# Kernel optimization log

Measured on AMD Instinct MI355X. Metric: run time of the kernel, lower is better.

The kernel has to match this reference:

```python
import jax, jax.numpy as jnp
from jax import lax
import numpy as np

B, S, G = 16, 384, 384
N = S + G
E_CHAR, D = 100, 128
H = D // 2              # LSTM hidden per direction
NHEAD, NHID = 4, 64
T = 21                  # crf_input_dim = label_alphabet.size() + 1
START, STOP = T - 2, T - 1
ALPHA = 0.2
CHAR_V, GAZ_V = 8000, 100000
NEG = -9e15             # pyGAT masked_fill value


def setup_inputs():
    key = jax.random.key(0)
    ks = jax.random.split(key, 20)
    f32 = jnp.float32
    def nrm(k, shape, s=0.05):
        return (jax.random.normal(k, shape) * s).astype(f32)
    eye = jnp.eye(N, dtype=bool)
    def adj(k):
        return ((jax.random.uniform(k, (B, N, N)) < 0.1) | eye[None]).astype(jnp.int32)
    return dict(
        batch_char=jax.random.randint(ks[0], (B, S), 0, CHAR_V),
        batch_len=jnp.full((B,), S, jnp.int32),
        gaz_list=jax.random.randint(ks[1], (B, G), 0, GAZ_V),
        t_graph=adj(ks[2]), c_graph=adj(ks[3]), l_graph=adj(ks[4]),
        mask=jnp.ones((B, S), jnp.int32),
        char_table=nrm(ks[5], (CHAR_V, E_CHAR)),
        gaz_table=nrm(ks[6], (GAZ_V, D)),
        w_ih_f=nrm(ks[7], (4 * H, E_CHAR)), w_hh_f=nrm(ks[8], (4 * H, H)),
        b_f=jnp.zeros((4 * H,), f32),
        w_ih_b=nrm(ks[9], (4 * H, E_CHAR)), w_hh_b=nrm(ks[10], (4 * H, H)),
        b_b=jnp.zeros((4 * H,), f32),
        h2h_W=nrm(ks[11], (T, D)), h2h_b=jnp.zeros((T,), f32),
        gat_Wh=nrm(ks[12], (3, NHEAD, D, NHID)),
        gat_ah=nrm(ks[13], (3, NHEAD, 2 * NHID)),
        gat_Wo=nrm(ks[14], (3, NHEAD * NHID, T)),
        gat_ao=nrm(ks[15], (3, 2 * T)),
        fuse_w=jnp.ones((4,), f32),
        transitions=nrm(ks[16], (T, T)),
    )


def _lstm_dir(x, w_ih, w_hh, b, reverse):
    # x: [B,S,E]; torch gate order i,f,g,o
    Bb = x.shape[0]
    Hh = w_hh.shape[1]
    xw = jnp.einsum('bse,ge->bsg', x, w_ih) + b
    def step(carry, xt):
        h, c = carry
        g = xt + h @ w_hh.T
        i, f, gg, o = jnp.split(g, 4, axis=-1)
        c = jax.nn.sigmoid(f) * c + jax.nn.sigmoid(i) * jnp.tanh(gg)
        h = jax.nn.sigmoid(o) * jnp.tanh(c)
        return (h, c), h
    h0 = jnp.zeros((Bb, Hh), x.dtype)
    _, hs = lax.scan(step, (h0, h0), xw.swapaxes(0, 1), reverse=reverse)
    return hs.swapaxes(0, 1)


def _gat_layer(x, adj, W, a, concat):
    # pyGAT batched layer: e_ij = LeakyReLU(a . [Wh_i || Wh_j]), masked softmax over j
    h = jnp.einsum('bnd,df->bnf', x, W)
    F_ = W.shape[1]
    f1 = h @ a[:F_]           # [B,N]
    f2 = h @ a[F_:]
    e = jax.nn.leaky_relu(f1[:, :, None] + f2[:, None, :], negative_slope=ALPHA)
    e = jnp.where(adj > 0, e, NEG)
    att = jax.nn.softmax(e, axis=-1)
    out = jnp.einsum('bij,bjf->bif', att, h)
    return jax.nn.elu(out) if concat else out


def _gat(x, adj, Wh, ah, Wo, ao):
    heads = jax.vmap(lambda W, a: _gat_layer(x, adj, W, a, True))(Wh, ah)  # [H,B,N,F]
    hcat = jnp.moveaxis(heads, 0, 2).reshape(x.shape[0], x.shape[1], -1)
    return jax.nn.elu(_gat_layer(hcat, adj, Wo, ao, False))


def _crf_feature(batch_char, gaz_list, graphs, char_table, gaz_table,
                 w_ih_f, w_hh_f, b_f, w_ih_b, w_hh_b, b_b, h2h_W, h2h_b,
                 gat_Wh, gat_ah, gat_Wo, gat_ao, fuse_w):
    emb = char_table[batch_char]                      # [B,S,E_CHAR]
    hf = _lstm_dir(emb, w_ih_f, w_hh_f, b_f, False)
    hb = _lstm_dir(emb, w_ih_b, w_hh_b, b_b, True)
    lstm_feat = jnp.concatenate([hf, hb], axis=-1)    # [B,S,D]
    gaz_feat = gaz_table[gaz_list]                    # [B,G,D]
    gat_in = jnp.concatenate([lstm_feat, gaz_feat], axis=1)  # [B,N,D]
    gat_outs = [_gat(gat_in, adj, gat_Wh[k], gat_ah[k], gat_Wo[k], gat_ao[k])[:, :S]
                for k, adj in enumerate(graphs)]
    lstm_proj = lstm_feat @ h2h_W.T + h2h_b           # [B,S,T]
    return (fuse_w[0] * lstm_proj + fuse_w[1] * gat_outs[0]
            + fuse_w[2] * gat_outs[1] + fuse_w[3] * gat_outs[2])


def _viterbi(feats, transitions, mask):
    Bb, Ss, Tt = feats.shape
    ids = jnp.arange(Tt)
    part0 = feats[:, 0, :] + transitions[START][None, :]
    def step(part, inp):
        feat_t, m_t = inp
        cur = part[:, :, None] + transitions[None] + feat_t[:, None, :]  # [B,prev,cur]
        new = cur.max(axis=1)
        bp = cur.argmax(axis=1)
        m = (m_t > 0)[:, None]
        return jnp.where(m, new, part), jnp.where(m, bp, ids[None, :])
    part, bps = lax.scan(step, part0,
                         (feats[:, 1:].swapaxes(0, 1), mask[:, 1:].swapaxes(0, 1)))
    last_tag = jnp.argmax(part + transitions[:, STOP][None, :], axis=1)
    def back(tag, bp):
        prev = jnp.take_along_axis(bp, tag[:, None], axis=1)[:, 0]
        return prev, prev
    _, prevs = lax.scan(back, last_tag, bps, reverse=True)   # prevs[j] = tag at time j
    return jnp.concatenate([prevs.swapaxes(0, 1), last_tag[:, None]], axis=1)


def reference(batch_char, batch_len, gaz_list, t_graph, c_graph, l_graph, mask,
              char_table, gaz_table, w_ih_f, w_hh_f, b_f, w_ih_b, w_hh_b, b_b,
              h2h_W, h2h_b, gat_Wh, gat_ah, gat_Wo, gat_ao, fuse_w, transitions):
    # batch_len is all == S (mask all ones), so packed BiLSTM == plain BiLSTM
    feats = _crf_feature(batch_char, gaz_list, (t_graph, c_graph, l_graph),
                         char_table, gaz_table, w_ih_f, w_hh_f, b_f,
                         w_ih_b, w_hh_b, b_b, h2h_W, h2h_b,
                         gat_Wh, gat_ah, gat_Wo, gat_ao, fuse_w)
    return _viterbi(feats, transitions, mask)
```

## Files before the change

### kernel.cpp

```cpp
#include <hip/hip_runtime.h>
#include <hip/hip_bf16.h>
#include <cstdint>
#include <cstddef>

#define BB 16
#define SS 384
#define GG 384
#define NN 768
#define DD 128
#define EC 100
#define TT 21
#define NHEADS 4
#define BN (BB*NN)
#define BS (BB*SS)

typedef float v2f __attribute__((ext_vector_type(2)));

__device__ __forceinline__ float sigf(float x) { return 1.0f / (1.0f + __expf(-x)); }
__device__ __forceinline__ float tanh_fast(float x) {
    return 1.0f - 2.0f / (__expf(2.0f * x) + 1.0f);
}
__device__ __forceinline__ float wred_max(float v) {
    #pragma unroll
    for (int o = 32; o > 0; o >>= 1) v = fmaxf(v, __shfl_xor(v, o));
    return v;
}
__device__ __forceinline__ float wred_sum(float v) {
    #pragma unroll
    for (int o = 32; o > 0; o >>= 1) v += __shfl_xor(v, o);
    return v;
}

__global__ __launch_bounds__(256) void k_xw(
    const int* __restrict__ batch_char, const float* __restrict__ char_table,
    const float* __restrict__ w_ih_f, const float* __restrict__ b_f,
    const float* __restrict__ w_ih_b, const float* __restrict__ b_b,
    float* __restrict__ xw_f, float* __restrict__ xw_b)
{
    __shared__ float At[EC * 68];
    __shared__ float Bt[EC * 68];
    __shared__ int   chs[64];
    const int tid = threadIdx.x;
    const int rt  = blockIdx.x;
    const int ot  = blockIdx.y;
    const int dir = ot >> 2, gt = ot & 3;
    const float* wih  = dir ? w_ih_b : w_ih_f;
    const float* bias = dir ? b_b    : b_f;
    float*       out  = dir ? xw_b   : xw_f;

    if (tid < 64) chs[tid] = batch_char[rt * 64 + tid];
    __syncthreads();
    for (int idx = tid; idx < 64 * EC; idx += 256) {
        int r = idx / EC, e = idx - r * EC;
        At[e * 68 + r] = char_table[(size_t)chs[r] * EC + e];
        Bt[e * 68 + r] = wih[(size_t)(gt * 64 + r) * EC + e];
    }
    __syncthreads();

    const int ty = tid >> 4, tx = tid & 15;
    const int r0 = ty * 4, c0 = tx * 4;
    float acc[4][4] = {};
    #pragma unroll 4
    for (int e = 0; e < EC; ++e) {
        float4 a = *(const float4*)&At[e * 68 + r0];
        float4 bv = *(const float4*)&Bt[e * 68 + c0];
        float av[4] = {a.x, a.y, a.z, a.w};
        float bb[4] = {bv.x, bv.y, bv.z, bv.w};
        #pragma unroll
        for (int i = 0; i < 4; ++i)
            #pragma unroll
            for (int j = 0; j < 4; ++j) acc[i][j] = fmaf(av[i], bb[j], acc[i][j]);
    }
    #pragma unroll
    for (int i = 0; i < 4; ++i) {
        int row = rt * 64 + r0 + i;
        int gc  = gt * 64 + c0;
        float4 o;
        o.x = acc[i][0] + bias[gc + 0];
        o.y = acc[i][1] + bias[gc + 1];
        o.z = acc[i][2] + bias[gc + 2];
        o.w = acc[i][3] + bias[gc + 3];
        *(float4*)&out[(size_t)row * 256 + gc] = o;
    }
}

__global__ __launch_bounds__(256) void k_gaz(
    const int* __restrict__ gaz_list, const float* __restrict__ gaz_table,
    float* __restrict__ gat_in)
{
    int idx = blockIdx.x * 256 + threadIdx.x;
    int d = idx & 127;
    int rest = idx >> 7;
    int g = rest % GG;
    int b = rest / GG;
    float v = gaz_table[(size_t)gaz_list[b * GG + g] * DD + d];
    gat_in[((size_t)b * NN + SS + g) * DD + d] = v;
}

__global__ __launch_bounds__(256) void k_lstm(
    const float* __restrict__ xw_f, const float* __restrict__ xw_b,
    const float* __restrict__ w_hh_f, const float* __restrict__ w_hh_b,
    float* __restrict__ gat_in)
{
    __shared__ float part[2][4][64][4];
    __shared__ float hbuf[4][64];
    const int tid = threadIdx.x, wv = tid >> 6, lane = tid & 63;
    const int b = blockIdx.x >> 1, dir = blockIdx.x & 1;
    const float* xw  = (dir ? xw_b : xw_f) + (size_t)b * SS * 256;
    const float* whh = dir ? w_hh_b : w_hh_f;
    v2f w2[4][8];
    #pragma unroll
    for (int g4 = 0; g4 < 4; ++g4) {
        const float* r = whh + (size_t)(g4 * 64 + lane) * 64 + 16 * wv;
        #pragma unroll
        for (int jj = 0; jj < 8; ++jj) w2[g4][jj] = v2f{r[2 * jj], r[2 * jj + 1]};
    }
    hbuf[wv][lane] = 0.f;
    float c = 0.f;
    int buf = 0;
    const int t0 = dir ? (SS - 1) : 0;
    float x0 = xw[t0 * 256 +   0 + lane];
    float x1 = xw[t0 * 256 +  64 + lane];
    float x2 = xw[t0 * 256 + 128 + lane];
    float x3 = xw[t0 * 256 + 192 + lane];
    const v2f* h2p = (const v2f*)&hbuf[wv][16 * wv];
    for (int tt = 0; tt < SS; ++tt) {
        const int t = dir ? (SS - 1 - tt) : tt;
        const int tn = dir ? (t - 1) : (t + 1);
        v2f a0 = v2f{0.f, 0.f}, a1 = v2f{0.f, 0.f}, a2 = v2f{0.f, 0.f}, a3 = v2f{0.f, 0.f};
        #pragma unroll
        for (int jj = 0; jj < 8; ++jj) {
            v2f hv = h2p[jj];
            a0 = __builtin_elementwise_fma(hv, w2[0][jj], a0);
            a1 = __builtin_elementwise_fma(hv, w2[1][jj], a1);
            a2 = __builtin_elementwise_fma(hv, w2[2][jj], a2);
            a3 = __builtin_elementwise_fma(hv, w2[3][jj], a3);
        }
        float4 pw;
        pw.x = a0.x + a0.y; pw.y = a1.x + a1.y;
        pw.z = a2.x + a2.y; pw.w = a3.x + a3.y;
        *(float4*)part[buf][wv][lane] = pw;
        float nx0 = 0.f, nx1 = 0.f, nx2 = 0.f, nx3 = 0.f;
        if (tt + 1 < SS) {
            nx0 = xw[tn * 256 +   0 + lane];
            nx1 = xw[tn * 256 +  64 + lane];
            nx2 = xw[tn * 256 + 128 + lane];
            nx3 = xw[tn * 256 + 192 + lane];
        }
        __syncthreads();
        float4 p0 = *(const float4*)part[buf][0][lane];
        float4 p1 = *(const float4*)part[buf][1][lane];
        float4 p2 = *(const float4*)part[buf][2][lane];
        float4 p3 = *(const float4*)part[buf][3][lane];
        float gi = ((p0.x + p1.x) + (p2.x + p3.x)) + x0;
        float gf = ((p0.y + p1.y) + (p2.y + p3.y)) + x1;
        float gg = ((p0.z + p1.z) + (p2.z + p3.z)) + x2;
        float go = ((p0.w + p1.w) + (p2.w + p3.w)) + x3;
        float nc = sigf(gf) * c + sigf(gi) * tanh_fast(gg);
        float nh = sigf(go) * tanh_fast(nc);
        c = nc;
        hbuf[wv][lane] = nh;
        if (wv == 0) gat_in[((size_t)b * NN + t) * DD + dir * 64 + lane] = nh;
        x0 = nx0; x1 = nx1; x2 = nx2; x3 = nx3;
        buf ^= 1;
    }
}

__global__ __launch_bounds__(256) void k_p1(
    const float* __restrict__ gat_in, const float* __restrict__ gat_Wh,
    const float* __restrict__ gat_ah, int k,
    float* __restrict__ h1, float* __restrict__ f1g, float* __restrict__ f2g)
{
    __shared__ float At[64 * 68];
    __shared__ float Bt[64 * 68];
    __shared__ float sf1[64], sf2[64];
    const int tid = threadIdx.x;
    const int rt = blockIdx.x, hd = blockIdx.y;
    if (tid < 64) { sf1[tid] = 0.f; sf2[tid] = 0.f; }
    const float* W = gat_Wh + ((size_t)(k * NHEADS + hd)) * DD * 64;
    const int ty = tid >> 4, tx = tid & 15;
    const int r0 = ty * 4, c0 = tx * 4;
    float acc[4][4] = {};
    for (int ph = 0; ph < 2; ++ph) {
        __syncthreads();
        for (int idx = tid; idx < 64 * 64; idx += 256) {
            int r = idx >> 6, e = idx & 63;
            At[e * 68 + r] = gat_in[((size_t)(rt * 64 + r)) * DD + ph * 64 + e];
            Bt[e * 68 + r] = W[(size_t)(ph * 64 + e) * 64 + r];
        }
        __syncthreads();
        #pragma unroll 4
        for (int e = 0; e < 64; ++e) {
            float4 a = *(const float4*)&At[e * 68 + r0];
            float4 bv = *(const float4*)&Bt[e * 68 + c0];
            float av[4] = {a.x, a.y, a.z, a.w};
            float bb[4] = {bv.x, bv.y, bv.z, bv.w};
            #pragma unroll
            for (int i = 0; i < 4; ++i)
                #pragma unroll
                for (int j = 0; j < 4; ++j) acc[i][j] = fmaf(av[i], bb[j], acc[i][j]);
        }
    }
    const float* ah = gat_ah + (size_t)(k * NHEADS + hd) * 128;
    float a1[4], a2[4];
    #pragma unroll
    for (int j = 0; j < 4; ++j) { a1[j] = ah[c0 + j]; a2[j] = ah[64 + c0 + j]; }
    #pragma unroll
    for (int i = 0; i < 4; ++i) {
        int n = rt * 64 + r0 + i;
        float4 o = make_float4(acc[i][0], acc[i][1], acc[i][2], acc[i][3]);
        *(float4*)&h1[((size_t)n * NHEADS + hd) * 64 + c0] = o;
        float p1 = acc[i][0] * a1[0] + acc[i][1] * a1[1] + acc[i][2] * a1[2] + acc[i][3] * a1[3];
        float p2 = acc[i][0] * a2[0] + acc[i][1] * a2[1] + acc[i][2] * a2[2] + acc[i][3] * a2[3];
        atomicAdd(&sf1[r0 + i], p1);
        atomicAdd(&sf2[r0 + i], p2);
    }
    __syncthreads();
    if (tid < 64) {
        f1g[hd * BN + rt * 64 + tid] = sf1[tid];
        f2g[hd * BN + rt * 64 + tid] = sf2[tid];
    }
}

__global__ __launch_bounds__(256) void k_attn1(
    const int* __restrict__ adj, const float* __restrict__ h1,
    const float* __restrict__ f1g, const float* __restrict__ f2g,
    float* __restrict__ out1, unsigned long long* __restrict__ packed)
{
    __shared__ int   nbr[NN];
    __shared__ float ep[NHEADS][NN];
    __shared__ unsigned long long wm[12];
    __shared__ int cntS;
    const int tid = threadIdx.x, wave = tid >> 6, lane = tid & 63;
    const int n = blockIdx.x;
    const int b = n / NN;
    #pragma unroll
    for (int it = 0; it < 3; ++it) {
        int j = it * 256 + tid;
        int a = adj[(size_t)n * NN + j];
        unsigned long long m = __ballot(a > 0);
        if (lane == 0) { wm[it * 4 + wave] = m; packed[(size_t)n * 12 + it * 4 + wave] = m; }
    }
    __syncthreads();
    if (wave == 0) {
        unsigned long long m = (lane < 12) ? wm[lane] : 0ULL;
        int pc = __popcll(m);
        int inc = pc;
        #pragma unroll
        for (int d = 1; d < 16; d <<= 1) { int t = __shfl_up(inc, d); if (lane >= d) inc += t; }
        int C = __shfl(inc, 11);
        if (lane == 0) cntS = C;
        int off = inc - pc;
        while (m) {
            int bit = __builtin_ctzll(m);
            nbr[off++] = lane * 64 + bit;
            m &= m - 1;
        }
    }
    __syncthreads();
    const int C = cntS;
    const int hd = wave;
    const float f1 = f1g[hd * BN + n];
    const float* f2p = f2g + hd * BN + b * NN;
    float mx = -3.0e38f;
    for (int t = lane; t < C; t += 64) {
        float e = f1 + f2p[nbr[t]];
        e = (e >= 0.f) ? e : 0.2f * e;
        ep[hd][t] = e;
        mx = fmaxf(mx, e);
    }
    mx = wred_max(mx);
    float sum = 0.f;
    for (int t = lane; t < C; t += 64) {
        float p = __expf(ep[hd][t] - mx);
        ep[hd][t] = p;
        sum += p;
    }
    sum = wred_sum(sum);
    const float* hb = h1 + (size_t)b * NN * (NHEADS * 64) + hd * 64 + lane;
    float ac0 = 0.f, ac1 = 0.f, ac2 = 0.f, ac3 = 0.f;
    int t = 0;
    for (; t + 3 < C; t += 4) {
        int j0 = nbr[t], j1 = nbr[t + 1], j2 = nbr[t + 2], j3 = nbr[t + 3];
        float p0 = ep[hd][t], p1 = ep[hd][t + 1], p2 = ep[hd][t + 2], p3 = ep[hd][t + 3];
        ac0 = fmaf(p0, hb[(size_t)j0 * 256], ac0);
        ac1 = fmaf(p1, hb[(size_t)j1 * 256], ac1);
        ac2 = fmaf(p2, hb[(size_t)j2 * 256], ac2);
        ac3 = fmaf(p3, hb[(size_t)j3 * 256], ac3);
    }
    for (; t < C; ++t) ac0 = fmaf(ep[hd][t], hb[(size_t)nbr[t] * 256], ac0);
    float r = ((ac0 + ac1) + (ac2 + ac3)) / sum;
    r = (r > 0.f) ? r : expm1f(r);
    out1[(size_t)n * 256 + hd * 64 + lane] = r;
}

__global__ __launch_bounds__(256) void k_p2(
    const float* __restrict__ out1, const float* __restrict__ gat_Wo,
    const float* __restrict__ gat_ao, int k,
    float* __restrict__ h2, float* __restrict__ f1o, float* __restrict__ f2o)
{
    __shared__ float ld[12 * 256];
    __shared__ float lf1[12], lf2[12];
    const int tid = threadIdx.x;
    const int blk = blockIdx.x;
    if (tid < 12) { lf1[tid] = 0.f; lf2[tid] = 0.f; }
    for (int idx = tid; idx < 12 * 256; idx += 256)
        ld[idx] = out1[(size_t)blk * 12 * 256 + idx];
    __syncthreads();
    if (tid < 252) {
        const int r = tid / TT, c = tid - r * TT;
        const float* Wo = gat_Wo + (size_t)k * 256 * TT;
        const float4* row4 = (const float4*)&ld[r * 256];
        float acc = 0.f;
        #pragma unroll 8
        for (int q4 = 0; q4 < 64; ++q4) {
            float4 v = row4[q4];
            int q = q4 * 4;
            acc = fmaf(v.x, Wo[(q + 0) * TT + c], acc);
            acc = fmaf(v.y, Wo[(q + 1) * TT + c], acc);
            acc = fmaf(v.z, Wo[(q + 2) * TT + c], acc);
            acc = fmaf(v.w, Wo[(q + 3) * TT + c], acc);
        }
        const int n = blk * 12 + r;
        h2[(size_t)n * TT + c] = acc;
        const float* ao = gat_ao + k * 2 * TT;
        atomicAdd(&lf1[r], acc * ao[c]);
        atomicAdd(&lf2[r], acc * ao[TT + c]);
    }
    __syncthreads();
    if (tid < 12) {
        f1o[blk * 12 + tid] = lf1[tid];
        f2o[blk * 12 + tid] = lf2[tid];
    }
}

__global__ __launch_bounds__(64) void k_attn2(
    const unsigned long long* __restrict__ packed,
    const float* __restrict__ h2, const float* __restrict__ f1o,
    const float* __restrict__ f2o, float* __restrict__ out2k)
{
    __shared__ int   nbr[NN];
    __shared__ float ep[NN];
    const int lane = threadIdx.x;
    const int blk = blockIdx.x;
    const int b = blk / SS, s = blk - b * SS;
    const int n = b * NN + s;
    unsigned long long w64 = (lane < 12) ? packed[(size_t)n * 12 + lane] : 0ULL;
    int pc = __popcll(w64);
    int inc = pc;
    #pragma unroll
    for (int d = 1; d < 16; d <<= 1) {
        int t = __shfl_up(inc, d, 16);
        if ((lane & 15) >= d) inc += t;
    }
    const int C = __shfl(inc, 11);
    int off = inc - pc;
    while (w64) {
        int bit = __builtin_ctzll(w64);
        nbr[off++] = lane * 64 + bit;
        w64 &= w64 - 1;
    }
    __syncthreads();
    const float f1 = f1o[n];
    const float* f2p = f2o + b * NN;
    float mx = -3.0e38f;
    for (int t = lane; t < C; t += 64) {
        int j = nbr[t];
        float e = f1 + f2p[j];
        e = (e >= 0.f) ? e : 0.2f * e;
        ep[t] = e;
        mx = fmaxf(mx, e);
    }
    mx = wred_max(mx);
    float sum = 0.f;
    for (int t = lane; t < C; t += 64) {
        float p = __expf(ep[t] - mx);
        ep[t] = p;
        sum += p;
    }
    sum = wred_sum(sum);
    const float* h2b = h2 + (size_t)b * NN * TT + ((lane < TT) ? lane : 0);
    float ac0 = 0.f, ac1 = 0.f, ac2 = 0.f, ac3 = 0.f;
    int t = 0;
    for (; t + 3 < C; t += 4) {
        int j0 = nbr[t], j1 = nbr[t + 1], j2 = nbr[t + 2], j3 = nbr[t + 3];
        float p0 = ep[t], p1 = ep[t + 1], p2 = ep[t + 2], p3 = ep[t + 3];
        ac0 = fmaf(p0, h2b[(size_t)j0 * TT], ac0);
        ac1 = fmaf(p1, h2b[(size_t)j1 * TT], ac1);
        ac2 = fmaf(p2, h2b[(size_t)j2 * TT], ac2);
        ac3 = fmaf(p3, h2b[(size_t)j3 * TT], ac3);
    }
    for (; t < C; ++t) ac0 = fmaf(ep[t], h2b[(size_t)nbr[t] * TT], ac0);
    if (lane < TT) {
        float r = ((ac0 + ac1) + (ac2 + ac3)) / sum;
        r = (r > 0.f) ? r : expm1f(r);
        out2k[(size_t)blk * TT + lane] = r;
    }
}

__global__ __launch_bounds__(64) void k_fuse(
    const float* __restrict__ gat_in, const float* __restrict__ h2h_W,
    const float* __restrict__ h2h_b, const float* __restrict__ fuse_w,
    const float* __restrict__ out2, float* __restrict__ feats)
{
    __shared__ float row[DD];
    const int lane = threadIdx.x;
    const int blk = blockIdx.x;
    const int b = blk / SS, s = blk - b * SS;
    const float* src = gat_in + ((size_t)b * NN + s) * DD;
    row[lane] = src[lane];
    row[lane + 64] = src[lane + 64];
    __syncthreads();
    if (lane < TT) {
        float acc = h2h_b[lane];
        const float4* w4 = (const float4*)&h2h_W[lane * DD];
        const float4* r4 = (const float4*)row;
        #pragma unroll 8
        for (int d4 = 0; d4 < 32; ++d4) {
            float4 w = w4[d4]; float4 v = r4[d4];
            acc = fmaf(w.x, v.x, acc); acc = fmaf(w.y, v.y, acc);
            acc = fmaf(w.z, v.z, acc); acc = fmaf(w.w, v.w, acc);
        }
        size_t o = (size_t)blk * TT + lane;
        feats[o] = fuse_w[0] * acc + fuse_w[1] * out2[o]
                 + fuse_w[2] * out2[(size_t)BS * TT + o]
                 + fuse_w[3] * out2[2 * (size_t)BS * TT + o];
    }
}

__global__ __launch_bounds__(64) void k_vit(
    const float* __restrict__ feats, const float* __restrict__ trans,
    int* __restrict__ out)
{
    __shared__ float part[24];
    __shared__ unsigned char bp[SS - 1][24];
    const int lane = threadIdx.x;
    const int b = blockIdx.x;
    const int pg = lane / TT;
    const int c = lane - pg * TT;
    const bool act = (pg < 3);
    const int p0 = pg * 7;
    float tc[7];
    if (act) {
        #pragma unroll
        for (int u = 0; u < 7; ++u) tc[u] = trans[(p0 + u) * TT + c];
    }
    if (lane < TT) part[lane] = feats[((size_t)b * SS) * TT + lane] + trans[19 * TT + lane];
    if (lane >= TT && lane < 24) part[lane] = -3.0e38f;
    __syncthreads();
    for (int t = 1; t < SS; ++t) {
        float best = -3.0e38f; int bi = 0;
        if (act) {
            #pragma unroll
            for (int u = 0; u < 7; ++u) {
                float v = part[p0 + u] + tc[u];
                if (v > best) { best = v; bi = p0 + u; }
            }
        }
        float bv1 = __shfl(best, lane + 21);
        int   bi1 = __shfl(bi,   lane + 21);
        float bv2 = __shfl(best, lane + 42);
        int   bi2 = __shfl(bi,   lane + 42);
        if (lane < TT) {
            if (bv1 > best) { best = bv1; bi = bi1; }
            if (bv2 > best) { best = bv2; bi = bi2; }
            bp[t - 1][lane] = (unsigned char)bi;
            part[lane] = best + feats[((size_t)b * SS + t) * TT + lane];
        }
        __syncthreads();
    }
    float fv = (lane < TT) ? part[lane] + trans[lane * TT + 20] : -3.0e38f;
    int fi = (lane < TT) ? lane : 0;
    #pragma unroll
    for (int o = 32; o > 0; o >>= 1) {
        float ov = __shfl_xor(fv, o);
        int oi = __shfl_xor(fi, o);
        if (ov > fv || (ov == fv && oi < fi)) { fv = ov; fi = oi; }
    }
    __syncthreads();
    if (lane == 0) {
        int cur = fi;
        out[b * SS + SS - 1] = cur;
        for (int u = SS - 2; u >= 0; --u) {
            cur = bp[u][cur];
            out[b * SS + u] = cur;
        }
    }
}

extern "C" void kernel_launch(void* const* d_in, const int* in_sizes, int n_in,
                              void* d_out, int out_size, void* d_ws, size_t ws_size,
                              hipStream_t stream) {
    (void)in_sizes; (void)n_in; (void)out_size; (void)ws_size;
    const int*   batch_char = (const int*)d_in[0];
    const int*   gaz_list   = (const int*)d_in[2];
    const int*   graphs[3]  = {(const int*)d_in[3], (const int*)d_in[4], (const int*)d_in[5]};
    const float* char_table = (const float*)d_in[7];
    const float* gaz_table  = (const float*)d_in[8];
    const float* w_ih_f = (const float*)d_in[9];
    const float* w_hh_f = (const float*)d_in[10];
    const float* b_f    = (const float*)d_in[11];
    const float* w_ih_b = (const float*)d_in[12];
    const float* w_hh_b = (const float*)d_in[13];
    const float* b_b    = (const float*)d_in[14];
    const float* h2h_W  = (const float*)d_in[15];
    const float* h2h_b  = (const float*)d_in[16];
    const float* gat_Wh = (const float*)d_in[17];
    const float* gat_ah = (const float*)d_in[18];
    const float* gat_Wo = (const float*)d_in[19];
    const float* gat_ao = (const float*)d_in[20];
    const float* fuse_w = (const float*)d_in[21];
    const float* trans  = (const float*)d_in[22];

    float* ws = (float*)d_ws;
    float* gat_in = ws;
    float* xw_f   = gat_in + 1572864;
    float* xw_b   = xw_f   + 1572864;
    float* h1     = xw_b   + 1572864;
    float* out1   = h1     + 3145728;
    float* h2     = out1   + 3145728;
    float* f1g    = h2     + 258048;
    float* f2g    = f1g    + 49152;
    float* f1o    = f2g    + 49152;
    float* f2o    = f1o    + 12288;
    float* out2   = f2o    + 12288;
    float* feats  = out2   + 387072;
    unsigned long long* packed = (unsigned long long*)(feats + 129024);

    k_xw<<<dim3(96, 8), 256, 0, stream>>>(batch_char, char_table, w_ih_f, b_f,
                                          w_ih_b, b_b, xw_f, xw_b);
    k_gaz<<<3072, 256, 0, stream>>>(gaz_list, gaz_table, gat_in);
    k_lstm<<<32, 256, 0, stream>>>(xw_f, xw_b, w_hh_f, w_hh_b, gat_in);
    for (int k = 0; k < 3; ++k) {
        k_p1<<<dim3(192, 4), 256, 0, stream>>>(gat_in, gat_Wh, gat_ah, k, h1, f1g, f2g);
        k_attn1<<<BN, 256, 0, stream>>>(graphs[k], h1, f1g, f2g, out1, packed);
        k_p2<<<1024, 256, 0, stream>>>(out1, gat_Wo, gat_ao, k, h2, f1o, f2o);
        k_attn2<<<BS, 64, 0, stream>>>(packed, h2, f1o, f2o, out2 + (size_t)k * BS * TT);
    }
    k_fuse<<<BS, 64, 0, stream>>>(gat_in, h2h_W, h2h_b, fuse_w, out2, feats);
    k_vit<<<BB, 64, 0, stream>>>(feats, trans, (int*)d_out);
}
```

Before: 948.6 us.

## Run LSTM recurrence in a single wavefront using readlane broadcasts

The BiLSTM recurrence kernel moves from four wavefronts that split the hidden-state dot product and combine partial sums through shared memory with a block barrier each step, to one 64-lane wavefront that holds all 256 recurrent weights per lane in registers. The hidden state is broadcast to all lanes with readlane, so the per-step LDS round trip and __syncthreads are gone. In exchange each lane does four times the FMAs per step plus 64 readlanes, and register use grows to about 256 VGPRs for weights, which could raise per-step latency on this serial critical path.

```diff
diff --git a/kernel.cpp b/kernel.cpp
--- a/kernel.cpp
+++ b/kernel.cpp
@@ -29,6 +29,9 @@
     #pragma unroll
     for (int o = 32; o > 0; o >>= 1) v += __shfl_xor(v, o);
     return v;
+}
+__device__ __forceinline__ float rlane(float v, int l) {
+    return __uint_as_float(__builtin_amdgcn_readlane(__float_as_uint(v), l));
 }
 
 __global__ __launch_bounds__(256) void k_xw(
@@ -97,49 +100,39 @@
     gat_in[((size_t)b * NN + SS + g) * DD + d] = v;
 }
 
-__global__ __launch_bounds__(256) void k_lstm(
+__global__ __launch_bounds__(64, 1) void k_lstm(
     const float* __restrict__ xw_f, const float* __restrict__ xw_b,
     const float* __restrict__ w_hh_f, const float* __restrict__ w_hh_b,
     float* __restrict__ gat_in)
 {
-    __shared__ float part[2][4][64][4];
-    __shared__ float hbuf[4][64];
-    const int tid = threadIdx.x, wv = tid >> 6, lane = tid & 63;
+    const int lane = threadIdx.x;
     const int b = blockIdx.x >> 1, dir = blockIdx.x & 1;
     const float* xw  = (dir ? xw_b : xw_f) + (size_t)b * SS * 256;
     const float* whh = dir ? w_hh_b : w_hh_f;
-    v2f w2[4][8];
-    #pragma unroll
-    for (int g4 = 0; g4 < 4; ++g4) {
-        const float* r = whh + (size_t)(g4 * 64 + lane) * 64 + 16 * wv;
+
+    v2f w2[4][32];
+    #pragma unroll
+    for (int g = 0; g < 4; ++g) {
+        const float4* r4 = (const float4*)(whh + (size_t)(g * 64 + lane) * 64);
         #pragma unroll
-        for (int jj = 0; jj < 8; ++jj) w2[g4][jj] = v2f{r[2 * jj], r[2 * jj + 1]};
-    }
-    hbuf[wv][lane] = 0.f;
-    float c = 0.f;
-    int buf = 0;
+        for (int q = 0; q < 16; ++q) {
+            float4 v = r4[q];
+            w2[g][2 * q]     = v2f{v.x, v.y};
+            w2[g][2 * q + 1] = v2f{v.z, v.w};
+        }
+    }
+
+    float h = 0.f, c = 0.f;
     const int t0 = dir ? (SS - 1) : 0;
     float x0 = xw[t0 * 256 +   0 + lane];
     float x1 = xw[t0 * 256 +  64 + lane];
     float x2 = xw[t0 * 256 + 128 + lane];
     float x3 = xw[t0 * 256 + 192 + lane];
-    const v2f* h2p = (const v2f*)&hbuf[wv][16 * wv];
+    float* outp = gat_in + ((size_t)b * NN) * DD + dir * 64 + lane;
+
     for (int tt = 0; tt < SS; ++tt) {
         const int t = dir ? (SS - 1 - tt) : tt;
         const int tn = dir ? (t - 1) : (t + 1);
-        v2f a0 = v2f{0.f, 0.f}, a1 = v2f{0.f, 0.f}, a2 = v2f{0.f, 0.f}, a3 = v2f{0.f, 0.f};
-        #pragma unroll
-        for (int jj = 0; jj < 8; ++jj) {
-            v2f hv = h2p[jj];
-            a0 = __builtin_elementwise_fma(hv, w2[0][jj], a0);
-            a1 = __builtin_elementwise_fma(hv, w2[1][jj], a1);
-            a2 = __builtin_elementwise_fma(hv, w2[2][jj], a2);
-            a3 = __builtin_elementwise_fma(hv, w2[3][jj], a3);
-        }
-        float4 pw;
-        pw.x = a0.x + a0.y; pw.y = a1.x + a1.y;
-        pw.z = a2.x + a2.y; pw.w = a3.x + a3.y;
-        *(float4*)part[buf][wv][lane] = pw;
         float nx0 = 0.f, nx1 = 0.f, nx2 = 0.f, nx3 = 0.f;
         if (tt + 1 < SS) {
             nx0 = xw[tn * 256 +   0 + lane];
@@ -147,22 +140,23 @@
             nx2 = xw[tn * 256 + 128 + lane];
             nx3 = xw[tn * 256 + 192 + lane];
         }
-        __syncthreads();
-        float4 p0 = *(const float4*)part[buf][0][lane];
-        float4 p1 = *(const float4*)part[buf][1][lane];
-        float4 p2 = *(const float4*)part[buf][2][lane];
-        float4 p3 = *(const float4*)part[buf][3][lane];
-        float gi = ((p0.x + p1.x) + (p2.x + p3.x)) + x0;
-        float gf = ((p0.y + p1.y) + (p2.y + p3.y)) + x1;
-        float gg = ((p0.z + p1.z) + (p2.z + p3.z)) + x2;
-        float go = ((p0.w + p1.w) + (p2.w + p3.w)) + x3;
+        v2f a0 = v2f{x0, 0.f}, a1 = v2f{x1, 0.f};
+        v2f a2 = v2f{x2, 0.f}, a3 = v2f{x3, 0.f};
+        #pragma unroll
+        for (int j = 0; j < 32; ++j) {
+            v2f hp = v2f{rlane(h, 2 * j), rlane(h, 2 * j + 1)};
+            a0 = __builtin_elementwise_fma(hp, w2[0][j], a0);
+            a1 = __builtin_elementwise_fma(hp, w2[1][j], a1);
+            a2 = __builtin_elementwise_fma(hp, w2[2][j], a2);
+            a3 = __builtin_elementwise_fma(hp, w2[3][j], a3);
+        }
+        float gi = a0.x + a0.y, gf = a1.x + a1.y;
+        float gg = a2.x + a2.y, go = a3.x + a3.y;
         float nc = sigf(gf) * c + sigf(gi) * tanh_fast(gg);
-        float nh = sigf(go) * tanh_fast(nc);
+        h = sigf(go) * tanh_fast(nc);
         c = nc;
-        hbuf[wv][lane] = nh;
-        if (wv == 0) gat_in[((size_t)b * NN + t) * DD + dir * 64 + lane] = nh;
+        outp[(size_t)t * DD] = h;
         x0 = nx0; x1 = nx1; x2 = nx2; x3 = nx3;
-        buf ^= 1;
     }
 }
 
@@ -530,7 +524,7 @@
     k_xw<<<dim3(96, 8), 256, 0, stream>>>(batch_char, char_table, w_ih_f, b_f,
                                           w_ih_b, b_b, xw_f, xw_b);
     k_gaz<<<3072, 256, 0, stream>>>(gaz_list, gaz_table, gat_in);
-    k_lstm<<<32, 256, 0, stream>>>(xw_f, xw_b, w_hh_f, w_hh_b, gat_in);
+    k_lstm<<<32, 64, 0, stream>>>(xw_f, xw_b, w_hh_f, w_hh_b, gat_in);
     for (int k = 0; k < 3; ++k) {
         k_p1<<<dim3(192, 4), 256, 0, stream>>>(gat_in, gat_Wh, gat_ah, k, h1, f1g, f2g);
         k_attn1<<<BN, 256, 0, stream>>>(graphs[k], h1, f1g, f2g, out1, packed);
```

Result: slower. 1.050 ms (+10.7%).

## Overlap LSTM with gaz gather and adjacency bit-packing in one kernel; register-resident Viterbi

Applied to the files above, without the earlier changes.

Merges the serial LSTM (32 blocks), the gaz embedding gather and the bit-packing of all three adjacency graphs into one launch. The packing and gather blocks can then fill the otherwise idle CUs while the long sequential LSTM runs, and k_attn1 reads the precomputed bitmasks instead of the raw int adjacency. Viterbi keeps its partial scores in registers exchanged by shuffles, prefetches the next feats row, and backtracks 16 steps at a time with readlane, removing block syncs and serial LDS chains. The packed buffer grows to three graphs, which needs more workspace.

```diff
diff --git a/kernel.cpp b/kernel.cpp
--- a/kernel.cpp
+++ b/kernel.cpp
@@ -14,6 +14,10 @@
 #define BN (BB*NN)
 #define BS (BB*SS)
 
+#define GAZ_BASE  32
+#define PACK_BASE (32 + 3072)
+#define PRE_GRID  (PACK_BASE + 3 * BN)
+
 typedef float v2f __attribute__((ext_vector_type(2)));
 
 __device__ __forceinline__ float sigf(float x) { return 1.0f / (1.0f + __expf(-x)); }
@@ -84,85 +88,100 @@
     }
 }
 
-__global__ __launch_bounds__(256) void k_gaz(
-    const int* __restrict__ gaz_list, const float* __restrict__ gaz_table,
-    float* __restrict__ gat_in)
-{
-    int idx = blockIdx.x * 256 + threadIdx.x;
-    int d = idx & 127;
-    int rest = idx >> 7;
-    int g = rest % GG;
-    int b = rest / GG;
-    float v = gaz_table[(size_t)gaz_list[b * GG + g] * DD + d];
-    gat_in[((size_t)b * NN + SS + g) * DD + d] = v;
-}
-
-__global__ __launch_bounds__(256) void k_lstm(
+__global__ __launch_bounds__(256) void k_pre(
     const float* __restrict__ xw_f, const float* __restrict__ xw_b,
     const float* __restrict__ w_hh_f, const float* __restrict__ w_hh_b,
-    float* __restrict__ gat_in)
+    float* __restrict__ gat_in,
+    const int* __restrict__ gaz_list, const float* __restrict__ gaz_table,
+    const int* __restrict__ adj0, const int* __restrict__ adj1,
+    const int* __restrict__ adj2, unsigned long long* __restrict__ packed)
 {
     __shared__ float part[2][4][64][4];
     __shared__ float hbuf[4][64];
-    const int tid = threadIdx.x, wv = tid >> 6, lane = tid & 63;
-    const int b = blockIdx.x >> 1, dir = blockIdx.x & 1;
-    const float* xw  = (dir ? xw_b : xw_f) + (size_t)b * SS * 256;
-    const float* whh = dir ? w_hh_b : w_hh_f;
-    v2f w2[4][8];
-    #pragma unroll
-    for (int g4 = 0; g4 < 4; ++g4) {
-        const float* r = whh + (size_t)(g4 * 64 + lane) * 64 + 16 * wv;
-        #pragma unroll
-        for (int jj = 0; jj < 8; ++jj) w2[g4][jj] = v2f{r[2 * jj], r[2 * jj + 1]};
-    }
-    hbuf[wv][lane] = 0.f;
-    float c = 0.f;
-    int buf = 0;
-    const int t0 = dir ? (SS - 1) : 0;
-    float x0 = xw[t0 * 256 +   0 + lane];
-    float x1 = xw[t0 * 256 +  64 + lane];
-    float x2 = xw[t0 * 256 + 128 + lane];
-    float x3 = xw[t0 * 256 + 192 + lane];
-    const v2f* h2p = (const v2f*)&hbuf[wv][16 * wv];
-    for (int tt = 0; tt < SS; ++tt) {
-        const int t = dir ? (SS - 1 - tt) : tt;
-        const int tn = dir ? (t - 1) : (t + 1);
-        v2f a0 = v2f{0.f, 0.f}, a1 = v2f{0.f, 0.f}, a2 = v2f{0.f, 0.f}, a3 = v2f{0.f, 0.f};
-        #pragma unroll
-        for (int jj = 0; jj < 8; ++jj) {
-            v2f hv = h2p[jj];
-            a0 = __builtin_elementwise_fma(hv, w2[0][jj], a0);
-            a1 = __builtin_elementwise_fma(hv, w2[1][jj], a1);
-            a2 = __builtin_elementwise_fma(hv, w2[2][jj], a2);
-            a3 = __builtin_elementwise_fma(hv, w2[3][jj], a3);
-        }
-        float4 pw;
-        pw.x = a0.x + a0.y; pw.y = a1.x + a1.y;
-        pw.z = a2.x + a2.y; pw.w = a3.x + a3.y;
-        *(float4*)part[buf][wv][lane] = pw;
-        float nx0 = 0.f, nx1 = 0.f, nx2 = 0.f, nx3 = 0.f;
-        if (tt + 1 < SS) {
-            nx0 = xw[tn * 256 +   0 + lane];
-            nx1 = xw[tn * 256 +  64 + lane];
-            nx2 = xw[tn * 256 + 128 + lane];
-            nx3 = xw[tn * 256 + 192 + lane];
-        }
-        __syncthreads();
-        float4 p0 = *(const float4*)part[buf][0][lane];
-        float4 p1 = *(const float4*)part[buf][1][lane];
-        float4 p2 = *(const float4*)part[buf][2][lane];
-        float4 p3 = *(const float4*)part[buf][3][lane];
-        float gi = ((p0.x + p1.x) + (p2.x + p3.x)) + x0;
-        float gf = ((p0.y + p1.y) + (p2.y + p3.y)) + x1;
-        float gg = ((p0.z + p1.z) + (p2.z + p3.z)) + x2;
-        float go = ((p0.w + p1.w) + (p2.w + p3.w)) + x3;
-        float nc = sigf(gf) * c + sigf(gi) * tanh_fast(gg);
-        float nh = sigf(go) * tanh_fast(nc);
-        c = nc;
-        hbuf[wv][lane] = nh;
-        if (wv == 0) gat_in[((size_t)b * NN + t) * DD + dir * 64 + lane] = nh;
-        x0 = nx0; x1 = nx1; x2 = nx2; x3 = nx3;
-        buf ^= 1;
+    const int bid = blockIdx.x;
+    const int tid = threadIdx.x;
+
+    if (bid < 32) {
+        const int wv = tid >> 6, lane = tid & 63;
+        const int b = bid >> 1, dir = bid & 1;
+        const float* xw  = (dir ? xw_b : xw_f) + (size_t)b * SS * 256;
+        const float* whh = dir ? w_hh_b : w_hh_f;
+        v2f w2[4][8];
+        #pragma unroll
+        for (int g4 = 0; g4 < 4; ++g4) {
+            const float* r = whh + (size_t)(g4 * 64 + lane) * 64 + 16 * wv;
+            #pragma unroll
+            for (int jj = 0; jj < 8; ++jj) w2[g4][jj] = v2f{r[2 * jj], r[2 * jj + 1]};
+        }
+        hbuf[wv][lane] = 0.f;
+        float c = 0.f;
+        int buf = 0;
+        const int t0 = dir ? (SS - 1) : 0;
+        float x0 = xw[t0 * 256 +   0 + lane];
+        float x1 = xw[t0 * 256 +  64 + lane];
+        float x2 = xw[t0 * 256 + 128 + lane];
+        float x3 = xw[t0 * 256 + 192 + lane];
+        const v2f* h2p = (const v2f*)&hbuf[wv][16 * wv];
+        for (int tt = 0; tt < SS; ++tt) {
+            const int t = dir ? (SS - 1 - tt) : tt;
+            const int tn = dir ? (t - 1) : (t + 1);
+            v2f a0 = v2f{0.f, 0.f}, a1 = v2f{0.f, 0.f}, a2 = v2f{0.f, 0.f}, a3 = v2f{0.f, 0.f};
+            #pragma unroll
+            for (int jj = 0; jj < 8; ++jj) {
+                v2f hv = h2p[jj];
+                a0 = __builtin_elementwise_fma(hv, w2[0][jj], a0);
+                a1 = __builtin_elementwise_fma(hv, w2[1][jj], a1);
+                a2 = __builtin_elementwise_fma(hv, w2[2][jj], a2);
+                a3 = __builtin_elementwise_fma(hv, w2[3][jj], a3);
+            }
+            float4 pw;
+            pw.x = a0.x + a0.y; pw.y = a1.x + a1.y;
+            pw.z = a2.x + a2.y; pw.w = a3.x + a3.y;
+            *(float4*)part[buf][wv][lane] = pw;
+            float nx0 = 0.f, nx1 = 0.f, nx2 = 0.f, nx3 = 0.f;
+            if (tt + 1 < SS) {
+                nx0 = xw[tn * 256 +   0 + lane];
+                nx1 = xw[tn * 256 +  64 + lane];
+                nx2 = xw[tn * 256 + 128 + lane];
+                nx3 = xw[tn * 256 + 192 + lane];
+            }
+            __syncthreads();
+            float4 p0 = *(const float4*)part[buf][0][lane];
+            float4 p1 = *(const float4*)part[buf][1][lane];
+            float4 p2 = *(const float4*)part[buf][2][lane];
+            float4 p3 = *(const float4*)part[buf][3][lane];
+            float gi = ((p0.x + p1.x) + (p2.x + p3.x)) + x0;
+            float gf = ((p0.y + p1.y) + (p2.y + p3.y)) + x1;
+            float gg = ((p0.z + p1.z) + (p2.z + p3.z)) + x2;
+            float go = ((p0.w + p1.w) + (p2.w + p3.w)) + x3;
+            float nc = sigf(gf) * c + sigf(gi) * tanh_fast(gg);
+            float nh = sigf(go) * tanh_fast(nc);
+            c = nc;
+            hbuf[wv][lane] = nh;
+            if (wv == 0) gat_in[((size_t)b * NN + t) * DD + dir * 64 + lane] = nh;
+            x0 = nx0; x1 = nx1; x2 = nx2; x3 = nx3;
+            buf ^= 1;
+        }
+    } else if (bid < PACK_BASE) {
+        int idx = (bid - GAZ_BASE) * 256 + tid;
+        int d = idx & 127;
+        int rest = idx >> 7;
+        int g = rest % GG;
+        int b = rest / GG;
+        float v = gaz_table[(size_t)gaz_list[b * GG + g] * DD + d];
+        gat_in[((size_t)b * NN + SS + g) * DD + d] = v;
+    } else {
+        const int row = bid - PACK_BASE;
+        const int k = row / BN, n = row - k * BN;
+        const int* adjk = (k == 0) ? adj0 : ((k == 1) ? adj1 : adj2);
+        const int wave = tid >> 6, lane = tid & 63;
+        #pragma unroll
+        for (int it = 0; it < 3; ++it) {
+            int j = it * 256 + tid;
+            unsigned long long m = __ballot(adjk[(size_t)n * NN + j] > 0);
+            if (lane == 0)
+                packed[((size_t)k * BN + n) * 12 + it * 4 + wave] = m;
+        }
     }
 }
 
@@ -223,27 +242,18 @@
 }
 
 __global__ __launch_bounds__(256) void k_attn1(
-    const int* __restrict__ adj, const float* __restrict__ h1,
+    const unsigned long long* __restrict__ packedk, const float* __restrict__ h1,
     const float* __restrict__ f1g, const float* __restrict__ f2g,
-    float* __restrict__ out1, unsigned long long* __restrict__ packed)
+    float* __restrict__ out1)
 {
     __shared__ int   nbr[NN];
     __shared__ float ep[NHEADS][NN];
-    __shared__ unsigned long long wm[12];
     __shared__ int cntS;
     const int tid = threadIdx.x, wave = tid >> 6, lane = tid & 63;
     const int n = blockIdx.x;
     const int b = n / NN;
-    #pragma unroll
-    for (int it = 0; it < 3; ++it) {
-        int j = it * 256 + tid;
-        int a = adj[(size_t)n * NN + j];
-        unsigned long long m = __ballot(a > 0);
-        if (lane == 0) { wm[it * 4 + wave] = m; packed[(size_t)n * 12 + it * 4 + wave] = m; }
-    }
-    __syncthreads();
     if (wave == 0) {
-        unsigned long long m = (lane < 12) ? wm[lane] : 0ULL;
+        unsigned long long m = (lane < 12) ? packedk[(size_t)n * 12 + lane] : 0ULL;
         int pc = __popcll(m);
         int inc = pc;
         #pragma unroll
@@ -335,7 +345,7 @@
 }
 
 __global__ __launch_bounds__(64) void k_attn2(
-    const unsigned long long* __restrict__ packed,
+    const unsigned long long* __restrict__ packedk,
     const float* __restrict__ h2, const float* __restrict__ f1o,
     const float* __restrict__ f2o, float* __restrict__ out2k)
 {
@@ -345,7 +355,7 @@
     const int blk = blockIdx.x;
     const int b = blk / SS, s = blk - b * SS;
     const int n = b * NN + s;
-    unsigned long long w64 = (lane < 12) ? packed[(size_t)n * 12 + lane] : 0ULL;
+    unsigned long long w64 = (lane < 12) ? packedk[(size_t)n * 12 + lane] : 0ULL;
     int pc = __popcll(w64);
     int inc = pc;
     #pragma unroll
@@ -432,7 +442,6 @@
     const float* __restrict__ feats, const float* __restrict__ trans,
     int* __restrict__ out)
 {
-    __shared__ float part[24];
     __shared__ unsigned char bp[SS - 1][24];
     const int lane = threadIdx.x;
     const int b = blockIdx.x;
@@ -445,15 +454,22 @@
         #pragma unroll
         for (int u = 0; u < 7; ++u) tc[u] = trans[(p0 + u) * TT + c];
     }
-    if (lane < TT) part[lane] = feats[((size_t)b * SS) * TT + lane] + trans[19 * TT + lane];
-    if (lane >= TT && lane < 24) part[lane] = -3.0e38f;
-    __syncthreads();
+    float pr = (lane < TT)
+        ? feats[((size_t)b * SS) * TT + lane] + trans[19 * TT + lane]
+        : -3.0e38f;
+    float nf = (lane < TT) ? feats[((size_t)b * SS + 1) * TT + lane] : 0.f;
     for (int t = 1; t < SS; ++t) {
+        float fcur = nf;
+        if (t + 1 < SS)
+            nf = (lane < TT) ? feats[((size_t)b * SS + t + 1) * TT + lane] : 0.f;
+        float pv[7];
+        #pragma unroll
+        for (int u = 0; u < 7; ++u) pv[u] = __shfl(pr, p0 + u);
         float best = -3.0e38f; int bi = 0;
         if (act) {
             #pragma unroll
             for (int u = 0; u < 7; ++u) {
-                float v = part[p0 + u] + tc[u];
+                float v = pv[u] + tc[u];
                 if (v > best) { best = v; bi = p0 + u; }
             }
         }
@@ -461,15 +477,14 @@
         int   bi1 = __shfl(bi,   lane + 21);
         float bv2 = __shfl(best, lane + 42);
         int   bi2 = __shfl(bi,   lane + 42);
+        if (bv1 > best) { best = bv1; bi = bi1; }
+        if (bv2 > best) { best = bv2; bi = bi2; }
         if (lane < TT) {
-            if (bv1 > best) { best = bv1; bi = bi1; }
-            if (bv2 > best) { best = bv2; bi = bi2; }
             bp[t - 1][lane] = (unsigned char)bi;
-            part[lane] = best + feats[((size_t)b * SS + t) * TT + lane];
-        }
-        __syncthreads();
-    }
-    float fv = (lane < TT) ? part[lane] + trans[lane * TT + 20] : -3.0e38f;
+            pr = best + fcur;
+        }
+    }
+    float fv = (lane < TT) ? pr + trans[lane * TT + 20] : -3.0e38f;
     int fi = (lane < TT) ? lane : 0;
     #pragma unroll
     for (int o = 32; o > 0; o >>= 1) {
@@ -477,14 +492,28 @@
         int oi = __shfl_xor(fi, o);
         if (ov > fv || (ov == fv && oi < fi)) { fv = ov; fi = oi; }
     }
-    __syncthreads();
-    if (lane == 0) {
-        int cur = fi;
-        out[b * SS + SS - 1] = cur;
-        for (int u = SS - 2; u >= 0; --u) {
-            cur = bp[u][cur];
-            out[b * SS + u] = cur;
-        }
+    int curs = __builtin_amdgcn_readfirstlane(fi);
+    if (lane == 0) out[b * SS + SS - 1] = curs;
+    int u = SS - 2;
+    int rem = (u + 1) & 15;
+    for (int i = 0; i < rem; ++i) {
+        int tag = bp[u][curs];
+        curs = __builtin_amdgcn_readfirstlane(tag);
+        if (lane == 0) out[b * SS + u] = curs;
+        --u;
+    }
+    const int ll = (lane < 24) ? lane : 0;
+    while (u >= 15) {
+        const int base = u - 15;
+        int v[16];
+        #pragma unroll
+        for (int i = 0; i < 16; ++i) v[i] = bp[base + i][ll];
+        #pragma unroll
+        for (int i = 15; i >= 0; --i) {
+            curs = __builtin_amdgcn_readlane(v[i], curs);
+            if (lane == 0) out[b * SS + base + i] = curs;
+        }
+        u = base - 1;
     }
 }
 
@@ -529,13 +558,15 @@
 
     k_xw<<<dim3(96, 8), 256, 0, stream>>>(batch_char, char_table, w_ih_f, b_f,
                                           w_ih_b, b_b, xw_f, xw_b);
-    k_gaz<<<3072, 256, 0, stream>>>(gaz_list, gaz_table, gat_in);
-    k_lstm<<<32, 256, 0, stream>>>(xw_f, xw_b, w_hh_f, w_hh_b, gat_in);
+    k_pre<<<PRE_GRID, 256, 0, stream>>>(xw_f, xw_b, w_hh_f, w_hh_b, gat_in,
+                                        gaz_list, gaz_table,
+                                        graphs[0], graphs[1], graphs[2], packed);
     for (int k = 0; k < 3; ++k) {
+        const unsigned long long* pk = packed + (size_t)k * BN * 12;
         k_p1<<<dim3(192, 4), 256, 0, stream>>>(gat_in, gat_Wh, gat_ah, k, h1, f1g, f2g);
-        k_attn1<<<BN, 256, 0, stream>>>(graphs[k], h1, f1g, f2g, out1, packed);
+        k_attn1<<<BN, 256, 0, stream>>>(pk, h1, f1g, f2g, out1);
         k_p2<<<1024, 256, 0, stream>>>(out1, gat_Wo, gat_ao, k, h2, f1o, f2o);
-        k_attn2<<<BS, 64, 0, stream>>>(packed, h2, f1o, f2o, out2 + (size_t)k * BS * TT);
+        k_attn2<<<BS, 64, 0, stream>>>(pk, h2, f1o, f2o, out2 + (size_t)k * BS * TT);
     }
     k_fuse<<<BS, 64, 0, stream>>>(gat_in, h2h_W, h2h_b, fuse_w, out2, feats);
     k_vit<<<BB, 64, 0, stream>>>(feats, trans, (int*)d_out);
```

Result: faster. 924.7 us (-2.5%).
